# Performance work log

Measured on AMD Instinct MI355X. Metric: run time of the kernel, lower is better.

The kernel has to match this reference:

```python
import jax, jax.numpy as jnp
import numpy as np

K = 3
STRIDE = 1
PAD = 1
DIL = 1


def _conv(x, w, b):
    # x: [B,C,H,W], w: [O,C,K,K] (OIHW)
    y = jax.lax.conv_general_dilated(
        x, w, window_strides=(STRIDE, STRIDE),
        padding=[(PAD, PAD), (PAD, PAD)],
        dimension_numbers=("NCHW", "OIHW", "NCHW"))
    return y + b[None, :, None, None]


def _bilinear(img, py, px):
    # img: [B,C,H,W]; py,px: [B,Ho,Wo] float sample coords; zero outside.
    B, C, H, W = img.shape
    y0 = jnp.floor(py)
    x0 = jnp.floor(px)
    wy = py - y0
    wx = px - x0

    def gather(yi, xi):
        valid = (yi >= 0) & (yi < H) & (xi >= 0) & (xi < W)
        yc = jnp.clip(yi, 0, H - 1).astype(jnp.int32)
        xc = jnp.clip(xi, 0, W - 1).astype(jnp.int32)
        v = jax.vmap(lambda im, yy, xx: im[:, yy, xx])(img, yc, xc)  # [B,C,Ho,Wo]
        return v * valid[:, None, :, :].astype(img.dtype)

    v00 = gather(y0, x0)
    v01 = gather(y0, x0 + 1)
    v10 = gather(y0 + 1, x0)
    v11 = gather(y0 + 1, x0 + 1)
    wy_ = wy[:, None]
    wx_ = wx[:, None]
    return ((1 - wy_) * (1 - wx_) * v00 + (1 - wy_) * wx_ * v01
            + wy_ * (1 - wx_) * v10 + wy_ * wx_ * v11)


def setup_inputs() -> dict:
    key = jax.random.key(0)
    ks = jax.random.split(key, 7)
    B, Cin, Cout, H, W = 16, 96, 96, 128, 128
    n = Cin * K * K
    stdv = 1.0 / np.sqrt(n)
    x = jax.random.normal(ks[0], (B, Cin, H, W), jnp.float32)
    weight = jax.random.uniform(ks[1], (Cout, Cin, K, K), jnp.float32, -stdv, stdv)
    bias = jnp.zeros((Cout,), jnp.float32)
    # offset/mask convs: small random weights so sampling offsets are nontrivial
    offset_w = jax.random.normal(ks[2], (2 * K * K, Cin, K, K), jnp.float32) * 0.01
    offset_b = jax.random.normal(ks[3], (2 * K * K,), jnp.float32) * 0.1
    mask_w = jax.random.normal(ks[4], (K * K, Cin, K, K), jnp.float32) * 0.01
    mask_b = jnp.zeros((K * K,), jnp.float32)
    return {"x": x, "weight": weight, "bias": bias,
            "offset_w": offset_w, "offset_b": offset_b,
            "mask_w": mask_w, "mask_b": mask_b}


def reference(x, weight, bias, offset_w, offset_b, mask_w, mask_b):
    offset = _conv(x, offset_w, offset_b)              # [B, 2*K*K, Ho, Wo]
    mask = jax.nn.sigmoid(_conv(x, mask_w, mask_b))    # [B, K*K, Ho, Wo]
    B, C, H, W = x.shape
    Ho, Wo = offset.shape[2], offset.shape[3]
    base_y = (jnp.arange(Ho) * STRIDE - PAD).astype(x.dtype)  # output-row base coord
    base_x = (jnp.arange(Wo) * STRIDE - PAD).astype(x.dtype)
    out = jnp.zeros((B, weight.shape[0], Ho, Wo), x.dtype)
    for k in range(K * K):  # fixed small loop over kernel taps
        i, j = k // K, k % K
        dy = offset[:, 2 * k]      # torchvision ordering: (dy, dx) per tap
        dx = offset[:, 2 * k + 1]
        py = base_y[None, :, None] + i * DIL + dy   # [B,Ho,Wo]
        px = base_x[None, None, :] + j * DIL + dx
        samp = _bilinear(x, py, px) * mask[:, k][:, None]  # [B,C,Ho,Wo]
        out = out + jnp.einsum("bchw,oc->bohw", samp, weight[:, :, i, j])
    return out + bias[None, :, None, None]
```

## Files before the change

### kernel.cpp

```cpp
#include <hip/hip_runtime.h>
#include <math.h>

#define W 128
#define H 128
#define HW 16384
#define CIN 96
#define COUT 96
#define BATCH 16
#define NPIX (BATCH * HW)
#define BPITCH 104
#define BTAP (COUT * BPITCH)
#define BSTG 10240
#define NOT (27 * 32 * 32)

typedef __bf16 bf16x8 __attribute__((ext_vector_type(8)));
typedef float f32x4 __attribute__((ext_vector_type(4)));
typedef unsigned int u32x4 __attribute__((ext_vector_type(4)));

typedef const unsigned int __attribute__((address_space(1))) gu32;
typedef unsigned int __attribute__((address_space(3))) lu32;
#define GLDS16(g, l) __builtin_amdgcn_global_load_lds((gu32*)(g), (lu32*)(l), 16, 0, 0)

__device__ inline float bflo(unsigned d) { union { unsigned u; float f; } t; t.u = d << 16; return t.f; }
__device__ inline float bfhi(unsigned d) { union { unsigned u; float f; } t; t.u = d & 0xffff0000u; return t.f; }

__global__ void prep_weights(const float* __restrict__ weight,
                             const float* __restrict__ offset_w,
                             const float* __restrict__ mask_w,
                             __bf16* __restrict__ wOT,
                             __bf16* __restrict__ wBTp) {
  int idx = blockIdx.x * blockDim.x + threadIdx.x;
  if (idx < NOT) {
    int c = idx & 31;
    int o = (idx >> 5) & 31;
    int ks = idx >> 10;
    int tap = ks / 3;
    int cg = (ks % 3) * 32 + c;
    float v = 0.f;
    if (o < 18)      v = offset_w[(o * CIN + cg) * 9 + tap];
    else if (o < 27) v = mask_w[((o - 18) * CIN + cg) * 9 + tap];
    wOT[idx] = (__bf16)v;
  } else {
    int j = idx - NOT;
    if (j < 9 * BTAP + 256) {
      int c = j % BPITCH;
      int o = (j / BPITCH) % COUT;
      int tap = j / BTAP;
      float v = 0.f;
      if (tap < 9 && c < CIN) v = weight[(o * CIN + c) * 9 + tap];
      wBTp[j] = (__bf16)v;
    }
  }
}

__global__ __launch_bounds__(256) void nhwc_kernel(const float* __restrict__ x,
                                                   __bf16* __restrict__ xT) {
  int tid = blockIdx.x * 256 + threadIdx.x;
  int b = tid >> 14, pix = tid & (HW - 1);
  const float* xp = x + (size_t)b * CIN * HW + pix;
  __bf16* op = xT + (size_t)tid * CIN;
#pragma unroll
  for (int c0 = 0; c0 < CIN; c0 += 8) {
    bf16x8 v;
#pragma unroll
    for (int j = 0; j < 8; ++j) v[j] = (__bf16)xp[(size_t)(c0 + j) * HW];
    *(bf16x8*)(op + c0) = v;
  }
}

#define OISS_TAP(TAP, G) {                                                    \
    int ki = (TAP) / 3, kj = (TAP) % 3;                                       \
    int yy = h + ki - 1, xx = wg + kj - 1;                                    \
    bool ok = ((unsigned)yy < (unsigned)H) && ((unsigned)xx < (unsigned)W);   \
    unsigned vo = ok ? (unsigned)((yy * W + xx) * 192) + choff : 0x7f000000u; \
    asm volatile("buffer_load_dwordx4 %0, %1, %2, %3 offen"                   \
                 : "=v"(G[0]) : "v"(vo), "s"(rsrcX), "s"(0));                 \
    asm volatile("buffer_load_dwordx4 %0, %1, %2, %3 offen"                   \
                 : "=v"(G[1]) : "v"(vo), "s"(rsrcX), "s"(64));                \
    asm volatile("buffer_load_dwordx4 %0, %1, %2, %3 offen"                   \
                 : "=v"(G[2]) : "v"(vo), "s"(rsrcX), "s"(128));               \
  }

#define OISS_B(TAP)                                                           \
  _Pragma("unroll") for (int s = 0; s < 3; ++s)                               \
  _Pragma("unroll") for (int nt = 0; nt < 2; ++nt)                            \
    asm volatile("buffer_load_dwordx4 %0, %1, %2, %3 offen"                   \
                 : "=v"(bb[s * 2 + nt])                                       \
                 : "v"(voffB), "s"(rsrcW),                                    \
                   "s"((TAP) * 6144 + s * 2048 + nt * 1024));

#define OCOMP(GC)                                                             \
  _Pragma("unroll") for (int s = 0; s < 3; ++s) {                             \
    bf16x8 a = __builtin_bit_cast(bf16x8, GC[s]);                             \
    acc[0] = __builtin_amdgcn_mfma_f32_16x16x32_bf16(                         \
        a, __builtin_bit_cast(bf16x8, bb[s * 2 + 0]), acc[0], 0, 0, 0);       \
    acc[1] = __builtin_amdgcn_mfma_f32_16x16x32_bf16(                         \
        a, __builtin_bit_cast(bf16x8, bb[s * 2 + 1]), acc[1], 0, 0, 0);       \
  }

__global__ __launch_bounds__(256) void offmask_mfma(
    const __bf16* __restrict__ xT, const __bf16* __restrict__ wOT,
    const float* __restrict__ offset_b, const float* __restrict__ mask_b,
    float* __restrict__ offm) {
  int t = threadIdx.x;
  int lane = t & 63;
  int wv = __builtin_amdgcn_readfirstlane(t >> 6);
  int ln15 = lane & 15;

  int bid = (int)blockIdx.x;
  int nb = (bid & 7) * 512 + (bid >> 3);
  int b = nb >> 8;
  int rem = nb & 255;
  int h = rem >> 1;
  int w0 = (rem & 1) << 6;

  int pl = (wv << 4) + ln15;
  int wg = w0 + pl;
  unsigned choff = (unsigned)((lane >> 4) << 4);

  const __bf16* xb = xT + (size_t)b * HW * CIN;

  unsigned long long ba = (unsigned long long)(const void*)xb;
  u32x4 rsrcX;
  rsrcX.x = (unsigned)ba; rsrcX.y = (unsigned)(ba >> 32);
  rsrcX.z = (unsigned)(HW * 192);
  rsrcX.w = 0x00020000u;
  unsigned long long bwo = (unsigned long long)(const void*)wOT;
  u32x4 rsrcW;
  rsrcW.x = (unsigned)bwo; rsrcW.y = (unsigned)(bwo >> 32);
  rsrcW.z = (unsigned)(NOT * 2);
  rsrcW.w = 0x00020000u;
  unsigned voffB = (unsigned)(ln15 * 64 + ((lane >> 4) << 4));

  f32x4 acc[2];
  acc[0] = (f32x4){0.f, 0.f, 0.f, 0.f};
  acc[1] = (f32x4){0.f, 0.f, 0.f, 0.f};

  u32x4 gA[3], gB[3], bb[6];

  OISS_TAP(0, gA);
#pragma unroll
  for (int tap = 0; tap < 9; ++tap) {
    OISS_B(tap);
    if (tap < 8) {
      if (tap & 1) { OISS_TAP(tap + 1, gA); } else { OISS_TAP(tap + 1, gB); }
      asm volatile("s_waitcnt vmcnt(3)" ::: "memory");
    } else {
      asm volatile("s_waitcnt vmcnt(0)" ::: "memory");
    }
    __builtin_amdgcn_sched_barrier(0);
    if (tap & 1) { OCOMP(gB); } else { OCOMP(gA); }
  }

  float* ob = offm + (size_t)b * 27 * HW + (size_t)h * W;
  int prow = w0 + (wv << 4) + ((lane >> 4) << 2);
  {
    float bv = offset_b[ln15];
    float4 o4;
    o4.x = acc[0][0] + bv; o4.y = acc[0][1] + bv;
    o4.z = acc[0][2] + bv; o4.w = acc[0][3] + bv;
    *(float4*)(ob + (size_t)ln15 * HW + prow) = o4;
  }
  if (ln15 < 11) {
    int o = 16 + ln15;
    bool sig = (o >= 18);
    float bv = sig ? mask_b[o - 18] : offset_b[o];
    float4 o4;
    float v0 = acc[1][0] + bv, v1 = acc[1][1] + bv;
    float v2 = acc[1][2] + bv, v3 = acc[1][3] + bv;
    if (sig) {
      v0 = 1.f / (1.f + expf(-v0)); v1 = 1.f / (1.f + expf(-v1));
      v2 = 1.f / (1.f + expf(-v2)); v3 = 1.f / (1.f + expf(-v3));
    }
    o4.x = v0; o4.y = v1; o4.z = v2; o4.w = v3;
    *(float4*)(ob + (size_t)o * HW + prow) = o4;
  }
}

#define GISS(K, G, WD) {                                                      \
    float dyv = (float)offt[2 * (K)][pl];                                     \
    float dxv = (float)offt[2 * (K) + 1][pl];                                 \
    float mv  = (float)offt[18 + (K)][pl];                                    \
    int ki = (K) / 3, kj = (K) % 3;                                           \
    float py = (float)(h - 1 + ki) + dyv;                                     \
    float px = (float)(wg - 1 + kj) + dxv;                                    \
    float fy = floorf(py), fx = floorf(px);                                   \
    float wyf = py - fy, wxf = px - fx;                                       \
    int iy0 = (int)fy, ix0 = (int)fx;                                         \
    int iy1 = iy0 + 1, ix1 = ix0 + 1;                                         \
    bool y0ok = (unsigned)iy0 < (unsigned)H;                                  \
    bool y1ok = (unsigned)iy1 < (unsigned)H;                                  \
    bool x0ok = (unsigned)ix0 < (unsigned)W;                                  \
    bool x1ok = (unsigned)ix1 < (unsigned)W;                                  \
    WD[0] = (y0ok && x0ok) ? (1.f - wyf) * (1.f - wxf) * mv : 0.f;            \
    WD[1] = (y0ok && x1ok) ? (1.f - wyf) * wxf * mv : 0.f;                    \
    WD[2] = (y1ok && x0ok) ? wyf * (1.f - wxf) * mv : 0.f;                    \
    WD[3] = (y1ok && x1ok) ? wyf * wxf * mv : 0.f;                            \
    int cy0 = min(max(iy0, 0), H - 1), cy1 = min(max(iy1, 0), H - 1);         \
    int cx0 = min(max(ix0, 0), W - 1), cx1 = min(max(ix1, 0), W - 1);         \
    unsigned v00 = (unsigned)((cy0 * W + cx0) * 192) + choff;                 \
    unsigned v01 = (unsigned)((cy0 * W + cx1) * 192) + choff;                 \
    unsigned v10 = (unsigned)((cy1 * W + cx0) * 192) + choff;                 \
    unsigned v11 = (unsigned)((cy1 * W + cx1) * 192) + choff;                 \
    _Pragma("unroll") for (int ks = 0; ks < 3; ++ks) {                        \
      asm volatile("buffer_load_dwordx4 %0, %1, %2, %3 offen"                 \
                   : "=v"(G[ks * 4 + 0]) : "v"(v00), "s"(rsrcX), "s"(ks * 64)); \
      asm volatile("buffer_load_dwordx4 %0, %1, %2, %3 offen"                 \
                   : "=v"(G[ks * 4 + 1]) : "v"(v01), "s"(rsrcX), "s"(ks * 64)); \
      asm volatile("buffer_load_dwordx4 %0, %1, %2, %3 offen"                 \
                   : "=v"(G[ks * 4 + 2]) : "v"(v10), "s"(rsrcX), "s"(ks * 64)); \
      asm volatile("buffer_load_dwordx4 %0, %1, %2, %3 offen"                 \
                   : "=v"(G[ks * 4 + 3]) : "v"(v11), "s"(rsrcX), "s"(ks * 64)); \
    } }

#define COMBINE_KS(G, KS, WV, AF)                                             \
  _Pragma("unroll") for (int j = 0; j < 8; ++j) {                             \
    unsigned d00 = G[(KS) * 4 + 0][j >> 1], d01 = G[(KS) * 4 + 1][j >> 1];    \
    unsigned d10 = G[(KS) * 4 + 2][j >> 1], d11 = G[(KS) * 4 + 3][j >> 1];    \
    float v00 = (j & 1) ? bfhi(d00) : bflo(d00);                              \
    float v01 = (j & 1) ? bfhi(d01) : bflo(d01);                              \
    float v10 = (j & 1) ? bfhi(d10) : bflo(d10);                              \
    float v11 = (j & 1) ? bfhi(d11) : bflo(d11);                              \
    AF[j] = (__bf16)(WV[0] * v00 + WV[1] * v01 + WV[2] * v10 + WV[3] * v11);  \
  }

#define STAGE_B(K) {                                                          \
    const __bf16* src = wBTp + (size_t)(K) * BTAP + (size_t)wv * 2560 +       \
                        (size_t)lane * 8;                                     \
    __bf16* dst = Blds + wv * 2560;                                           \
    _Pragma("unroll") for (int q = 0; q < 5; ++q)                             \
      GLDS16(src + q * 512, dst + q * 512);                                   \
  }

__global__ __launch_bounds__(256, 3) void deform_kernel(
    const __bf16* __restrict__ xT, const float* __restrict__ offm,
    const __bf16* __restrict__ wBTp, const float* __restrict__ bias,
    float* __restrict__ out) {
  __shared__ alignas(16) __bf16 Blds[BSTG];
  __shared__ __bf16 offt[27][64];

  int t = threadIdx.x;
  int lane = t & 63;
  int wv = __builtin_amdgcn_readfirstlane(t >> 6);
  int ln15 = lane & 15;

  int bid = (int)blockIdx.x;
  int nb = (bid & 7) * 512 + (bid >> 3);
  int b = nb >> 8;
  int rem = nb & 255;
  int h = rem >> 1;
  int w0 = (rem & 1) << 6;

  int pl = (wv << 4) + ln15;
  int wg = w0 + pl;
  unsigned choff = (unsigned)((lane >> 4) << 4);

  const __bf16* xb = xT + (size_t)b * HW * CIN;
  const float* ob = offm + (size_t)b * 27 * HW;

  unsigned long long ba = (unsigned long long)(const void*)xb;
  u32x4 rsrcX;
  rsrcX.x = (unsigned)ba; rsrcX.y = (unsigned)(ba >> 32);
  rsrcX.z = 0xffffffffu;  rsrcX.w = 0x00020000u;

  for (int e = t; e < 27 * 64; e += 256) {
    int o = e >> 6, p = e & 63;
    offt[o][p] = (__bf16)ob[(size_t)o * HW + (size_t)h * W + w0 + p];
  }
  __syncthreads();

  f32x4 acc[6];
#pragma unroll
  for (int nt = 0; nt < 6; ++nt) acc[nt] = (f32x4){0.f, 0.f, 0.f, 0.f};

  u32x4 g[12];
  f32x4 wd;
  const __bf16* bfrag = Blds + (size_t)ln15 * BPITCH + ((lane >> 4) << 3);

  GISS(0, g, wd);
  STAGE_B(0);

  for (int k = 0; k < 9; ++k) {
    asm volatile("s_waitcnt vmcnt(5)" ::: "memory");
    __builtin_amdgcn_sched_barrier(0);

    bf16x8 af0, af1, af2;
    COMBINE_KS(g, 0, wd, af0);
    COMBINE_KS(g, 1, wd, af1);
    COMBINE_KS(g, 2, wd, af2);

    __syncthreads();

    if (k < 8) { GISS(k + 1, g, wd); }

#pragma unroll
    for (int nt = 0; nt < 6; ++nt) {
      const __bf16* bp = bfrag + nt * 16 * BPITCH;
      bf16x8 b0 = *(const bf16x8*)(bp);
      bf16x8 b1 = *(const bf16x8*)(bp + 32);
      bf16x8 b2 = *(const bf16x8*)(bp + 64);
      acc[nt] = __builtin_amdgcn_mfma_f32_16x16x32_bf16(af0, b0, acc[nt], 0, 0, 0);
      acc[nt] = __builtin_amdgcn_mfma_f32_16x16x32_bf16(af1, b1, acc[nt], 0, 0, 0);
      acc[nt] = __builtin_amdgcn_mfma_f32_16x16x32_bf16(af2, b2, acc[nt], 0, 0, 0);
    }

    if (k < 8) {
      __syncthreads();
      STAGE_B(k + 1);
    }
  }

  float* outb = out + (size_t)b * COUT * HW + (size_t)h * W;
  int prow = w0 + (wv << 4) + ((lane >> 4) << 2);
#pragma unroll
  for (int nt = 0; nt < 6; ++nt) {
    int ch = nt * 16 + ln15;
    float bv = bias[ch];
    float4 o4;
    o4.x = acc[nt][0] + bv;
    o4.y = acc[nt][1] + bv;
    o4.z = acc[nt][2] + bv;
    o4.w = acc[nt][3] + bv;
    *(float4*)(outb + (size_t)ch * HW + prow) = o4;
  }
}

extern "C" void kernel_launch(void* const* d_in, const int* in_sizes, int n_in,
                              void* d_out, int out_size, void* d_ws, size_t ws_size,
                              hipStream_t stream) {
  const float* x        = (const float*)d_in[0];
  const float* weight   = (const float*)d_in[1];
  const float* bias     = (const float*)d_in[2];
  const float* offset_w = (const float*)d_in[3];
  const float* offset_b = (const float*)d_in[4];
  const float* mask_w   = (const float*)d_in[5];
  const float* mask_b   = (const float*)d_in[6];
  float* out = (float*)d_out;

  __bf16* xT   = (__bf16*)d_ws;
  float*  offm = (float*)(xT + (size_t)NPIX * CIN);
  __bf16* wOT  = (__bf16*)(offm + (size_t)BATCH * 27 * HW);
  __bf16* wBTp = wOT + NOT;

  const int nPrep = NOT + 9 * BTAP + 256;
  prep_weights<<<(nPrep + 255) / 256, 256, 0, stream>>>(weight, offset_w, mask_w, wOT, wBTp);
  nhwc_kernel<<<NPIX / 256, 256, 0, stream>>>(x, xT);
  offmask_mfma<<<BATCH * H * (W / 64), 256, 0, stream>>>(xT, wOT, offset_b, mask_b, offm);
  deform_kernel<<<BATCH * H * (W / 64), 256, 0, stream>>>(xT, offm, wBTp, bias, out);
}
```

Baseline: 285.1 us.

## Fuse offset/mask conv into deformable conv kernel via shared memory

Merges the offset/mask MFMA convolution kernel into the deformable sampling kernel. Each block computes its own 27 offset/mask channels for its 64-pixel row segment and writes them directly into the shared offt table, instead of round-tripping through a global fp32 buffer. This removes one kernel launch and the global write and read of the offset/mask tensor. In exchange the occupancy hint drops from 3 to 2 blocks per SM, and the offset phase now runs serially before the sampling phase inside each block.

```diff
diff --git a/kernel.cpp b/kernel.cpp
--- a/kernel.cpp
+++ b/kernel.cpp
@@ -92,90 +92,11 @@
 #define OCOMP(GC)                                                             \
   _Pragma("unroll") for (int s = 0; s < 3; ++s) {                             \
     bf16x8 a = __builtin_bit_cast(bf16x8, GC[s]);                             \
-    acc[0] = __builtin_amdgcn_mfma_f32_16x16x32_bf16(                         \
-        a, __builtin_bit_cast(bf16x8, bb[s * 2 + 0]), acc[0], 0, 0, 0);       \
-    acc[1] = __builtin_amdgcn_mfma_f32_16x16x32_bf16(                         \
-        a, __builtin_bit_cast(bf16x8, bb[s * 2 + 1]), acc[1], 0, 0, 0);       \
-  }
-
-__global__ __launch_bounds__(256) void offmask_mfma(
-    const __bf16* __restrict__ xT, const __bf16* __restrict__ wOT,
-    const float* __restrict__ offset_b, const float* __restrict__ mask_b,
-    float* __restrict__ offm) {
-  int t = threadIdx.x;
-  int lane = t & 63;
-  int wv = __builtin_amdgcn_readfirstlane(t >> 6);
-  int ln15 = lane & 15;
-
-  int bid = (int)blockIdx.x;
-  int nb = (bid & 7) * 512 + (bid >> 3);
-  int b = nb >> 8;
-  int rem = nb & 255;
-  int h = rem >> 1;
-  int w0 = (rem & 1) << 6;
-
-  int pl = (wv << 4) + ln15;
-  int wg = w0 + pl;
-  unsigned choff = (unsigned)((lane >> 4) << 4);
-
-  const __bf16* xb = xT + (size_t)b * HW * CIN;
-
-  unsigned long long ba = (unsigned long long)(const void*)xb;
-  u32x4 rsrcX;
-  rsrcX.x = (unsigned)ba; rsrcX.y = (unsigned)(ba >> 32);
-  rsrcX.z = (unsigned)(HW * 192);
-  rsrcX.w = 0x00020000u;
-  unsigned long long bwo = (unsigned long long)(const void*)wOT;
-  u32x4 rsrcW;
-  rsrcW.x = (unsigned)bwo; rsrcW.y = (unsigned)(bwo >> 32);
-  rsrcW.z = (unsigned)(NOT * 2);
-  rsrcW.w = 0x00020000u;
-  unsigned voffB = (unsigned)(ln15 * 64 + ((lane >> 4) << 4));
-
-  f32x4 acc[2];
-  acc[0] = (f32x4){0.f, 0.f, 0.f, 0.f};
-  acc[1] = (f32x4){0.f, 0.f, 0.f, 0.f};
-
-  u32x4 gA[3], gB[3], bb[6];
-
-  OISS_TAP(0, gA);
-#pragma unroll
-  for (int tap = 0; tap < 9; ++tap) {
-    OISS_B(tap);
-    if (tap < 8) {
-      if (tap & 1) { OISS_TAP(tap + 1, gA); } else { OISS_TAP(tap + 1, gB); }
-      asm volatile("s_waitcnt vmcnt(3)" ::: "memory");
-    } else {
-      asm volatile("s_waitcnt vmcnt(0)" ::: "memory");
-    }
-    __builtin_amdgcn_sched_barrier(0);
-    if (tap & 1) { OCOMP(gB); } else { OCOMP(gA); }
-  }
-
-  float* ob = offm + (size_t)b * 27 * HW + (size_t)h * W;
-  int prow = w0 + (wv << 4) + ((lane >> 4) << 2);
-  {
-    float bv = offset_b[ln15];
-    float4 o4;
-    o4.x = acc[0][0] + bv; o4.y = acc[0][1] + bv;
-    o4.z = acc[0][2] + bv; o4.w = acc[0][3] + bv;
-    *(float4*)(ob + (size_t)ln15 * HW + prow) = o4;
-  }
-  if (ln15 < 11) {
-    int o = 16 + ln15;
-    bool sig = (o >= 18);
-    float bv = sig ? mask_b[o - 18] : offset_b[o];
-    float4 o4;
-    float v0 = acc[1][0] + bv, v1 = acc[1][1] + bv;
-    float v2 = acc[1][2] + bv, v3 = acc[1][3] + bv;
-    if (sig) {
-      v0 = 1.f / (1.f + expf(-v0)); v1 = 1.f / (1.f + expf(-v1));
-      v2 = 1.f / (1.f + expf(-v2)); v3 = 1.f / (1.f + expf(-v3));
-    }
-    o4.x = v0; o4.y = v1; o4.z = v2; o4.w = v3;
-    *(float4*)(ob + (size_t)o * HW + prow) = o4;
-  }
-}
+    oacc[0] = __builtin_amdgcn_mfma_f32_16x16x32_bf16(                        \
+        a, __builtin_bit_cast(bf16x8, bb[s * 2 + 0]), oacc[0], 0, 0, 0);      \
+    oacc[1] = __builtin_amdgcn_mfma_f32_16x16x32_bf16(                        \
+        a, __builtin_bit_cast(bf16x8, bb[s * 2 + 1]), oacc[1], 0, 0, 0);      \
+  }
 
 #define GISS(K, G, WD) {                                                      \
     float dyv = (float)offt[2 * (K)][pl];                                     \
@@ -232,10 +153,11 @@
       GLDS16(src + q * 512, dst + q * 512);                                   \
   }
 
-__global__ __launch_bounds__(256, 3) void deform_kernel(
-    const __bf16* __restrict__ xT, const float* __restrict__ offm,
-    const __bf16* __restrict__ wBTp, const float* __restrict__ bias,
-    float* __restrict__ out) {
+__global__ __launch_bounds__(256, 2) void fused_kernel(
+    const __bf16* __restrict__ xT, const __bf16* __restrict__ wOT,
+    const __bf16* __restrict__ wBTp,
+    const float* __restrict__ offset_b, const float* __restrict__ mask_b,
+    const float* __restrict__ bias, float* __restrict__ out) {
   __shared__ alignas(16) __bf16 Blds[BSTG];
   __shared__ __bf16 offt[27][64];
 
@@ -256,16 +178,58 @@
   unsigned choff = (unsigned)((lane >> 4) << 4);
 
   const __bf16* xb = xT + (size_t)b * HW * CIN;
-  const float* ob = offm + (size_t)b * 27 * HW;
 
   unsigned long long ba = (unsigned long long)(const void*)xb;
   u32x4 rsrcX;
   rsrcX.x = (unsigned)ba; rsrcX.y = (unsigned)(ba >> 32);
-  rsrcX.z = 0xffffffffu;  rsrcX.w = 0x00020000u;
-
-  for (int e = t; e < 27 * 64; e += 256) {
-    int o = e >> 6, p = e & 63;
-    offt[o][p] = (__bf16)ob[(size_t)o * HW + (size_t)h * W + w0 + p];
+  rsrcX.z = (unsigned)(HW * 192);
+  rsrcX.w = 0x00020000u;
+  unsigned long long bwo = (unsigned long long)(const void*)wOT;
+  u32x4 rsrcW;
+  rsrcW.x = (unsigned)bwo; rsrcW.y = (unsigned)(bwo >> 32);
+  rsrcW.z = (unsigned)(NOT * 2);
+  rsrcW.w = 0x00020000u;
+  unsigned voffB = (unsigned)(ln15 * 64 + ((lane >> 4) << 4));
+
+  int prow_l = (wv << 4) + ((lane >> 4) << 2);
+
+  {
+    f32x4 oacc[2];
+    oacc[0] = (f32x4){0.f, 0.f, 0.f, 0.f};
+    oacc[1] = (f32x4){0.f, 0.f, 0.f, 0.f};
+    u32x4 gA[3], gB[3], bb[6];
+
+    OISS_TAP(0, gA);
+#pragma unroll
+    for (int tap = 0; tap < 9; ++tap) {
+      OISS_B(tap);
+      if (tap < 8) {
+        if (tap & 1) { OISS_TAP(tap + 1, gA); } else { OISS_TAP(tap + 1, gB); }
+        asm volatile("s_waitcnt vmcnt(3)" ::: "memory");
+      } else {
+        asm volatile("s_waitcnt vmcnt(0)" ::: "memory");
+      }
+      __builtin_amdgcn_sched_barrier(0);
+      if (tap & 1) { OCOMP(gB); } else { OCOMP(gA); }
+    }
+
+    {
+      float bv = offset_b[ln15];
+#pragma unroll
+      for (int r = 0; r < 4; ++r)
+        offt[ln15][prow_l + r] = (__bf16)(oacc[0][r] + bv);
+    }
+    if (ln15 < 11) {
+      int o = 16 + ln15;
+      bool sig = (o >= 18);
+      float bv = sig ? mask_b[o - 18] : offset_b[o];
+#pragma unroll
+      for (int r = 0; r < 4; ++r) {
+        float v = oacc[1][r] + bv;
+        if (sig) v = 1.f / (1.f + expf(-v));
+        offt[o][prow_l + r] = (__bf16)v;
+      }
+    }
   }
   __syncthreads();
 
@@ -311,7 +275,7 @@
   }
 
   float* outb = out + (size_t)b * COUT * HW + (size_t)h * W;
-  int prow = w0 + (wv << 4) + ((lane >> 4) << 2);
+  int prow = w0 + prow_l;
 #pragma unroll
   for (int nt = 0; nt < 6; ++nt) {
     int ch = nt * 16 + ln15;
@@ -338,13 +302,12 @@
   float* out = (float*)d_out;
 
   __bf16* xT   = (__bf16*)d_ws;
-  float*  offm = (float*)(xT + (size_t)NPIX * CIN);
-  __bf16* wOT  = (__bf16*)(offm + (size_t)BATCH * 27 * HW);
+  __bf16* wOT  = xT + (size_t)NPIX * CIN;
   __bf16* wBTp = wOT + NOT;
 
   const int nPrep = NOT + 9 * BTAP + 256;
   prep_weights<<<(nPrep + 255) / 256, 256, 0, stream>>>(weight, offset_w, mask_w, wOT, wBTp);
   nhwc_kernel<<<NPIX / 256, 256, 0, stream>>>(x, xT);
-  offmask_mfma<<<BATCH * H * (W / 64), 256, 0, stream>>>(xT, wOT, offset_b, mask_b, offm);
-  deform_kernel<<<BATCH * H * (W / 64), 256, 0, stream>>>(xT, offm, wBTp, bias, out);
+  fused_kernel<<<BATCH * H * (W / 64), 256, 0, stream>>>(
+      xT, wOT, wBTp, offset_b, mask_b, bias, out);
 }
```

Measured after the change: 260.5 us. -8.6%, faster.
